# Kernel optimization log

Measured on AMD Instinct MI355X. Metric: run time of the kernel, lower is better.

## Reference

```python
import jax, jax.numpy as jnp
import numpy as np


def setup_inputs() -> dict:
    key = jax.random.key(0)
    ks = jax.random.split(key, 7)
    O, I, K = 64, 64, 3
    D = K * K
    x = jax.random.normal(ks[0], (32, I, 224, 224), jnp.float32)
    weight_loc = jax.random.normal(ks[1], (O, I, K, K), jnp.float32) * 0.05
    weight_L = jax.random.normal(ks[2], (O, I, D, D), jnp.float32) * 0.05
    bias_loc = jax.random.normal(ks[3], (O,), jnp.float32) * 0.05
    bias_ro = jax.random.normal(ks[4], (O,), jnp.float32) * 0.05
    eps_w = jax.random.normal(ks[5], (O, I, D), jnp.float32)
    eps_b = jax.random.normal(ks[6], (O,), jnp.float32)
    return {"x": x, "weight_loc": weight_loc, "weight_L": weight_L,
            "bias_loc": bias_loc, "bias_ro": bias_ro,
            "eps_w": eps_w, "eps_b": eps_b}


def reference(x, weight_loc, weight_L, bias_loc, bias_ro, eps_w, eps_b):
    # weight_loc: [O, I, K, K]; weight_L: [O, I, D, D] with D = K*K
    O, I, K, _ = weight_loc.shape
    D = K * K
    # diag_softplus: softplus on the diagonal of each per-(o,i) scale_tril,
    # keep strictly-lower part; MVN uses the lower-triangular scale_tril.
    diag = jnp.diagonal(weight_L, axis1=-2, axis2=-1)            # [O, I, D]
    eye = jnp.eye(D, dtype=weight_L.dtype)
    L = jnp.tril(weight_L, -1) + jax.nn.softplus(diag)[..., None] * eye  # [O, I, D, D]
    # Batched MVN rsample: loc + L @ eps, collapsing the O*I Python loop
    w = weight_loc + jnp.einsum('oiab,oib->oia', L, eps_w).reshape(O, I, K, K)
    # Bias rsample: loc + eps * softplus(ro)
    b = bias_loc + eps_b * jax.nn.softplus(bias_ro)              # [O]
    out = jax.lax.conv_general_dilated(
        x, w, window_strides=(1, 1), padding='SAME',
        dimension_numbers=('NCHW', 'OIHW', 'NCHW'))
    return out + b[None, :, None, None]
```

## Files before the change

### kernel.cpp

```cpp
#include <hip/hip_runtime.h>
#include <hip/hip_bf16.h>
#include <stdint.h>

typedef short bhalf8 __attribute__((ext_vector_type(8)));
typedef float facc4 __attribute__((ext_vector_type(4)));

static __device__ __forceinline__ unsigned short f2bfu(float f) {
  return __builtin_bit_cast(unsigned short, __float2bfloat16(f));
}

__global__ void prep_kernel(const float* __restrict__ wloc,
                            const float* __restrict__ wL,
                            const float* __restrict__ eps_w,
                            const float* __restrict__ bloc,
                            const float* __restrict__ bro,
                            const float* __restrict__ eps_b,
                            short* __restrict__ wt, float* __restrict__ bias,
                            short* __restrict__ zeros) {
  int t = blockIdx.x * 256 + threadIdx.x;
  int o = t >> 6, i = t & 63;
  int kc = i >> 5, il = i & 31;
  const float* Lp = wL + (size_t)t * 81;
  const float* ep = eps_w + (size_t)t * 9;
  const float* lp = wloc + (size_t)t * 9;
  float e[9];
#pragma unroll
  for (int b = 0; b < 9; ++b) e[b] = ep[b];
#pragma unroll
  for (int a = 0; a < 9; ++a) {
    float s = lp[a];
    for (int b = 0; b < a; ++b) s += Lp[a * 9 + b] * e[b];
    float d = Lp[a * 9 + a];
    float sp = (d > 20.f) ? d : log1pf(expf(d));
    s += sp * e[a];
    wt[((a * 2 + kc) * 64 + o) * 32 + il] = (short)f2bfu(s);
  }
  if (t < 64) {
    float d = bro[t];
    float sp = (d > 20.f) ? d : log1pf(expf(d));
    bias[t] = bloc[t] + eps_b[t] * sp;
  }
  if (t < 16) zeros[t] = 0;
}

__global__ __launch_bounds__(512) void to_nhwc_kernel(
    const float* __restrict__ x, short* __restrict__ xh) {
  int b = blockIdx.x;
  int n = b / 196;
  int p0 = (b % 196) * 256;
  int t = threadIdx.x;
  int pl = t >> 3, c8 = t & 7;
  const float* xp = x + (size_t)(n * 64 + c8 * 8) * 50176 + p0 + pl * 4;
  short* op = xh + ((size_t)n * 50176 + p0 + pl * 4) * 64 + c8 * 8;
  float4 v[8];
#pragma unroll
  for (int j = 0; j < 8; ++j) v[j] = *(const float4*)(xp + (size_t)j * 50176);
#pragma unroll
  for (int s = 0; s < 4; ++s) {
    bhalf8 h;
#pragma unroll
    for (int j = 0; j < 8; ++j) h[j] = f2bfu(((const float*)&v[j])[s]);
    *(bhalf8*)(op + s * 64) = h;
  }
}

__global__ __launch_bounds__(512, 4) void conv_awt_kernel(
    const short* __restrict__ xh, const short* __restrict__ wtg,
    const float* __restrict__ bias, const short* __restrict__ zeros,
    float* __restrict__ out) {
  extern __shared__ short smem[];
  short* lds_x = smem;
  short* lds_w = smem + 21120;

  int b0 = blockIdx.x;
  int b = (b0 & 7) * 448 + (b0 >> 3);
  int ht = b % 28;
  int rest = b / 28;
  int w4 = rest & 3, n = rest >> 2;
  int h0 = ht * 8, w0 = w4 * 64;
  int t = threadIdx.x, lane = t & 63, wv = t >> 6;
  int l15 = lane & 15, l4 = lane >> 4;

  facc4 acc[4][4];
#pragma unroll
  for (int om = 0; om < 4; ++om)
#pragma unroll
    for (int p = 0; p < 4; ++p) {
      facc4 z = {0.f, 0.f, 0.f, 0.f};
      acc[om][p] = z;
    }

  const size_t nbase = (size_t)n * 50176 * 64;
  for (int ic = 0; ic < 2; ++ic) {
#pragma unroll
    for (int k = 0; k < 6; ++k) {
      int id = k * 512 + t;
      if (id < 2640) {
        int cc = id % 66;
        int rg = id / 66;
        int g = rg & 3, r = rg >> 2;
        int h_in = h0 - 1 + r, w_in = w0 - 1 + cc;
        const short* src =
            (h_in >= 0 && h_in < 224 && w_in >= 0 && w_in < 224)
                ? xh + nbase + (size_t)(h_in * 224 + w_in) * 64 + ic * 32 +
                      g * 8
                : zeros;
        __builtin_amdgcn_global_load_lds(
            (const __attribute__((address_space(1))) void*)src,
            (__attribute__((address_space(3))) void*)((char*)lds_x +
                                                      (k * 512 + wv * 64) *
                                                          16),
            16, 0, 0);
      }
    }
#pragma unroll
    for (int k = 0; k < 5; ++k) {
      int w = k * 512 + t;
      if (w < 2304) {
        const short* src = wtg + (w >> 8) * 4096 + ic * 2048 + (w & 255) * 8;
        __builtin_amdgcn_global_load_lds(
            (const __attribute__((address_space(1))) void*)src,
            (__attribute__((address_space(3))) void*)((char*)lds_w +
                                                      (k * 512 + wv * 64) *
                                                          16),
            16, 0, 0);
      }
    }
    __syncthreads();
#pragma unroll
    for (int kh = 0; kh < 3; ++kh) {
      int r = wv + kh;
#pragma unroll
      for (int kw = 0; kw < 3; ++kw) {
        const int tap = kh * 3 + kw;
        const short* ab = lds_w + tap * 2048 + l15 * 32 + (l4 << 3);
        bhalf8 a[4];
#pragma unroll
        for (int om = 0; om < 4; ++om)
          a[om] = *(const bhalf8*)(ab + om * 512);
#pragma unroll
        for (int p = 0; p < 4; ++p) {
          int tc = p * 16 + l15 + kw;
          bhalf8 bv = *(const bhalf8*)(lds_x + (((r * 4 + l4) * 66) + tc) * 8);
#pragma unroll
          for (int om = 0; om < 4; ++om)
            acc[om][p] = __builtin_amdgcn_mfma_f32_16x16x32_bf16(
                a[om], bv, acc[om][p], 0, 0, 0);
        }
      }
    }
    if (ic == 0) __syncthreads();
  }

  int h = h0 + wv;
#pragma unroll
  for (int om = 0; om < 4; ++om) {
#pragma unroll
    for (int jj = 0; jj < 4; ++jj) {
      int o = om * 16 + l4 * 4 + jj;
      float bo = bias[o];
      float* op = out + ((size_t)(n * 64 + o) * 224 + h) * 224 + w0;
#pragma unroll
      for (int p = 0; p < 4; ++p) {
        int wg = w0 + p * 16 + l15;
        if (wg < 224) op[p * 16 + l15] = acc[om][p][jj] + bo;
      }
    }
  }
}

typedef unsigned int uintv2 __attribute__((ext_vector_type(2)));
#define LD1(cj, i)                                                   \
  ((hok && (w_in0 + (i)) >= 0 && (w_in0 + (i)) < 224)                \
       ? cbase[(size_t)(cj) * 50176 + w_in0 + (i)]                   \
       : 0.f)

__global__ __launch_bounds__(256, 4) void conv_onepass_kernel(
    const float* __restrict__ x, const short* __restrict__ wt,
    const float* __restrict__ bias, float* __restrict__ out) {
  __shared__ short lds[6 * 66 * 32];
  int b0 = blockIdx.x;
  int b = (b0 & 7) * 896 + (b0 >> 3);
  int ht = b % 56;
  int rest = b / 56;
  int w4 = rest & 3, n = rest >> 2;
  int h0 = ht * 4, w0 = w4 * 64;
  int t = threadIdx.x, lane = t & 63, wv = t >> 6;
  int l15 = lane & 15, l4 = lane >> 4;

  facc4 acc[4][4];
#pragma unroll
  for (int om = 0; om < 4; ++om)
#pragma unroll
    for (int p = 0; p < 4; ++p) {
      facc4 z = {0.f, 0.f, 0.f, 0.f};
      acc[om][p] = z;
    }

  for (int ic = 0; ic < 2; ++ic) {
#pragma unroll
    for (int k = 0; k < 4; ++k) {
      int u = t + k * 256;
      if (u < 816) {
        int chg = u & 7;
        int tmp = u >> 3;
        int ccg = tmp % 17, r = tmp / 17;
        int h_in = h0 - 1 + r;
        bool hok = (h_in >= 0) & (h_in < 224);
        int w_in0 = w0 - 1 + ccg * 4;
        int ch0 = ic * 32 + chg * 4;
        const float* cbase =
            x + ((size_t)(n * 64 + ch0) * 224 + (hok ? h_in : 0)) * 224;
        float4 v0, v1, v2, v3;
        if (hok && w_in0 >= 0 && w_in0 + 3 < 224) {
          v0 = *(const float4*)(cbase + w_in0);
          v1 = *(const float4*)(cbase + 50176 + w_in0);
          v2 = *(const float4*)(cbase + 2 * 50176 + w_in0);
          v3 = *(const float4*)(cbase + 3 * 50176 + w_in0);
        } else {
          v0 = make_float4(LD1(0, 0), LD1(0, 1), LD1(0, 2), LD1(0, 3));
          v1 = make_float4(LD1(1, 0), LD1(1, 1), LD1(1, 2), LD1(1, 3));
          v2 = make_float4(LD1(2, 0), LD1(2, 1), LD1(2, 2), LD1(2, 3));
          v3 = make_float4(LD1(3, 0), LD1(3, 1), LD1(3, 2), LD1(3, 3));
        }
        int g = chg >> 1;
        int halfsel = (chg & 1) << 2;
#pragma unroll
        for (int i = 0; i < 4; ++i) {
          int cc = ccg * 4 + i;
          if (cc < 66) {
            float a0 = ((const float*)&v0)[i], a1 = ((const float*)&v1)[i];
            float a2 = ((const float*)&v2)[i], a3 = ((const float*)&v3)[i];
            unsigned int w0p =
                (unsigned int)f2bfu(a0) | ((unsigned int)f2bfu(a1) << 16);
            unsigned int w1p =
                (unsigned int)f2bfu(a2) | ((unsigned int)f2bfu(a3) << 16);
            int addr =
                (r * 66 + cc) * 32 + ((g ^ ((cc >> 1) & 3)) << 3) + halfsel;
            uintv2 pk = {w0p, w1p};
            *(uintv2*)(lds + addr) = pk;
          }
        }
      }
    }
    __syncthreads();
#pragma unroll
    for (int kh = 0; kh < 3; ++kh) {
      int r = wv + kh;
#pragma unroll
      for (int kw = 0; kw < 3; ++kw) {
        const short* wb =
            wt + (((kh * 3 + kw) * 2 + ic) * 64 + l15) * 32 + (l4 << 3);
        bhalf8 a[4];
#pragma unroll
        for (int om = 0; om < 4; ++om)
          a[om] = *(const bhalf8*)(wb + om * 512);
#pragma unroll
        for (int p = 0; p < 4; ++p) {
          int tc = p * 16 + l15 + kw;
          bhalf8 bv = *(const bhalf8*)(lds + (r * 66 + tc) * 32 +
                                       ((l4 ^ ((tc >> 1) & 3)) << 3));
#pragma unroll
          for (int om = 0; om < 4; ++om)
            acc[om][p] = __builtin_amdgcn_mfma_f32_16x16x32_bf16(
                a[om], bv, acc[om][p], 0, 0, 0);
        }
      }
    }
    if (ic == 0) __syncthreads();
  }

  int h = h0 + wv;
#pragma unroll
  for (int om = 0; om < 4; ++om) {
#pragma unroll
    for (int j = 0; j < 4; ++j) {
      int o = om * 16 + l4 * 4 + j;
      float bo = bias[o];
      float* op = out + ((size_t)(n * 64 + o) * 224 + h) * 224 + w0;
#pragma unroll
      for (int p = 0; p < 4; ++p) {
        int wg = w0 + p * 16 + l15;
        if (wg < 224) op[p * 16 + l15] = acc[om][p][j] + bo;
      }
    }
  }
}

extern "C" void kernel_launch(void* const* d_in, const int* in_sizes, int n_in,
                              void* d_out, int out_size, void* d_ws,
                              size_t ws_size, hipStream_t stream) {
  const float* x = (const float*)d_in[0];
  const float* wloc = (const float*)d_in[1];
  const float* wL = (const float*)d_in[2];
  const float* bloc = (const float*)d_in[3];
  const float* bro = (const float*)d_in[4];
  const float* eps_w = (const float*)d_in[5];
  const float* eps_b = (const float*)d_in[6];
  float* outp = (float*)d_out;

  short* wt = (short*)d_ws;
  float* bias = (float*)((char*)d_ws + 73728);
  short* zeros = (short*)((char*)d_ws + 73984);
  short* xh = (short*)((char*)d_ws + 74240);
  const size_t need = 74240ull + (size_t)32 * 50176 * 64 * 2;

  prep_kernel<<<16, 256, 0, stream>>>(wloc, wL, eps_w, bloc, bro, eps_b, wt,
                                      bias, zeros);
  if (ws_size >= need) {
    to_nhwc_kernel<<<32 * 196, 512, 0, stream>>>(x, xh);
    const int dyn_lds = (21120 + 18432) * 2;
    hipFuncSetAttribute((const void*)conv_awt_kernel,
                        hipFuncAttributeMaxDynamicSharedMemorySize, dyn_lds);
    conv_awt_kernel<<<3584, 512, dyn_lds, stream>>>(xh, wt, bias, zeros, outp);
  } else {
    conv_onepass_kernel<<<7168, 256, 0, stream>>>(x, wt, bias, outp);
  }
}
```

Measured before the change: 343.6 us.

## Double-buffer conv input/weight staging in LDS across four channel chunks

```diff
diff --git a/kernel.cpp b/kernel.cpp
--- a/kernel.cpp
+++ b/kernel.cpp
@@ -3,6 +3,7 @@
 #include <stdint.h>
 
 typedef short bhalf8 __attribute__((ext_vector_type(8)));
+typedef short bhalf4 __attribute__((ext_vector_type(4)));
 typedef float facc4 __attribute__((ext_vector_type(4)));
 
 static __device__ __forceinline__ unsigned short f2bfu(float f) {
@@ -19,7 +20,6 @@
                             short* __restrict__ zeros) {
   int t = blockIdx.x * 256 + threadIdx.x;
   int o = t >> 6, i = t & 63;
-  int kc = i >> 5, il = i & 31;
   const float* Lp = wL + (size_t)t * 81;
   const float* ep = eps_w + (size_t)t * 9;
   const float* lp = wloc + (size_t)t * 9;
@@ -33,7 +33,7 @@
     float d = Lp[a * 9 + a];
     float sp = (d > 20.f) ? d : log1pf(expf(d));
     s += sp * e[a];
-    wt[((a * 2 + kc) * 64 + o) * 32 + il] = (short)f2bfu(s);
+    wt[((a * 8 + (i >> 3)) * 64 + o) * 8 + (i & 7)] = (short)f2bfu(s);
   }
   if (t < 64) {
     float d = bro[t];
@@ -64,7 +64,7 @@
   }
 }
 
-__global__ __launch_bounds__(512, 4) void conv_awt_kernel(
+__global__ __launch_bounds__(512, 4) void conv_pipe_kernel(
     const short* __restrict__ xh, const short* __restrict__ wtg,
     const float* __restrict__ bias, const short* __restrict__ zeros,
     float* __restrict__ out) {
@@ -80,6 +80,59 @@
   int h0 = ht * 8, w0 = w4 * 64;
   int t = threadIdx.x, lane = t & 63, wv = t >> 6;
   int l15 = lane & 15, l4 = lane >> 4;
+  int gA = l4 >> 1, sub4 = (l4 & 1) * 4;
+
+  const int cxbase = wv * 165;
+  const int cwbase = wv * 144;
+  int pre_px[3];
+#pragma unroll
+  for (int k = 0; k < 3; ++k) {
+    int id = cxbase + k * 64 + lane;
+    if (id >= 1320) id = 0;
+    int cc = id % 66;
+    int rg = id / 66;
+    int g = rg & 1, r = rg >> 1;
+    int h_in = h0 - 1 + r, w_in = w0 - 1 + cc;
+    bool ok = (h_in >= 0) & (h_in < 224) & (w_in >= 0) & (w_in < 224);
+    pre_px[k] = ok ? ((h_in * 224 + w_in) * 64 + g * 8) : -1;
+  }
+  int pre_wt[3];
+#pragma unroll
+  for (int k = 0; k < 3; ++k) {
+    int id = cwbase + k * 64 + lane;
+    if (id >= 1152) id = 0;
+    int a = id >> 7, rem = id & 127;
+    int g = rem >> 6, o = rem & 63;
+    pre_wt[k] = (a * 512 + g * 64 + o) * 8;
+  }
+  const size_t nbase = (size_t)n * 50176 * 64;
+
+#define STAGE(qq)                                                          \
+  do {                                                                     \
+    const int q_ = (qq);                                                   \
+    const short* gx_ = xh + nbase + q_ * 16;                               \
+    short* lx_ = lds_x + (q_ & 1) * 10560 + cxbase * 8;                    \
+    _Pragma("unroll") for (int k = 0; k < 3; ++k) {                        \
+      if (k * 64 + lane < 165) {                                           \
+        const short* src = (pre_px[k] >= 0) ? gx_ + pre_px[k] : zeros;     \
+        __builtin_amdgcn_global_load_lds(                                  \
+            (const __attribute__((address_space(1))) void*)src,            \
+            (__attribute__((address_space(3))) void*)(lx_ + k * 512), 16,  \
+            0, 0);                                                         \
+      }                                                                    \
+    }                                                                      \
+    const short* gw_ = wtg + q_ * 1024;                                    \
+    short* lw_ = lds_w + (q_ & 1) * 9216 + cwbase * 8;                     \
+    _Pragma("unroll") for (int k = 0; k < 3; ++k) {                        \
+      if (k * 64 + lane < 144) {                                           \
+        __builtin_amdgcn_global_load_lds(                                  \
+            (const __attribute__((address_space(1))) void*)(gw_ +          \
+                                                            pre_wt[k]),    \
+            (__attribute__((address_space(3))) void*)(lw_ + k * 512), 16,  \
+            0, 0);                                                         \
+      }                                                                    \
+    }                                                                      \
+  } while (0)
 
   facc4 acc[4][4];
 #pragma unroll
@@ -90,67 +143,49 @@
       acc[om][p] = z;
     }
 
-  const size_t nbase = (size_t)n * 50176 * 64;
-  for (int ic = 0; ic < 2; ++ic) {
-#pragma unroll
-    for (int k = 0; k < 6; ++k) {
-      int id = k * 512 + t;
-      if (id < 2640) {
-        int cc = id % 66;
-        int rg = id / 66;
-        int g = rg & 3, r = rg >> 2;
-        int h_in = h0 - 1 + r, w_in = w0 - 1 + cc;
-        const short* src =
-            (h_in >= 0 && h_in < 224 && w_in >= 0 && w_in < 224)
-                ? xh + nbase + (size_t)(h_in * 224 + w_in) * 64 + ic * 32 +
-                      g * 8
-                : zeros;
-        __builtin_amdgcn_global_load_lds(
-            (const __attribute__((address_space(1))) void*)src,
-            (__attribute__((address_space(3))) void*)((char*)lds_x +
-                                                      (k * 512 + wv * 64) *
-                                                          16),
-            16, 0, 0);
-      }
-    }
-#pragma unroll
-    for (int k = 0; k < 5; ++k) {
-      int w = k * 512 + t;
-      if (w < 2304) {
-        const short* src = wtg + (w >> 8) * 4096 + ic * 2048 + (w & 255) * 8;
-        __builtin_amdgcn_global_load_lds(
-            (const __attribute__((address_space(1))) void*)src,
-            (__attribute__((address_space(3))) void*)((char*)lds_w +
-                                                      (k * 512 + wv * 64) *
-                                                          16),
-            16, 0, 0);
-      }
-    }
-    __syncthreads();
+  STAGE(0);
+#pragma unroll
+  for (int q = 0; q < 4; ++q) {
+    if (q < 3) STAGE(q + 1);
+    __builtin_amdgcn_sched_barrier(0);
+    if (q < 3)
+      asm volatile("s_waitcnt vmcnt(6)" ::: "memory");
+    else
+      asm volatile("s_waitcnt vmcnt(0)" ::: "memory");
+    __builtin_amdgcn_sched_barrier(0);
+    __builtin_amdgcn_s_barrier();
+    __builtin_amdgcn_sched_barrier(0);
+
+    const short* bx = lds_x + (q & 1) * 10560;
+    const short* bw = lds_w + (q & 1) * 9216;
 #pragma unroll
     for (int kh = 0; kh < 3; ++kh) {
       int r = wv + kh;
 #pragma unroll
       for (int kw = 0; kw < 3; ++kw) {
-        const int tap = kh * 3 + kw;
-        const short* ab = lds_w + tap * 2048 + l15 * 32 + (l4 << 3);
-        bhalf8 a[4];
+        const int a = kh * 3 + kw;
+        bhalf4 av[4];
 #pragma unroll
         for (int om = 0; om < 4; ++om)
-          a[om] = *(const bhalf8*)(ab + om * 512);
+          av[om] = *(const bhalf4*)(bw + ((a * 2 + gA) * 64 + om * 16 + l15) *
+                                             8 +
+                                    sub4);
 #pragma unroll
         for (int p = 0; p < 4; ++p) {
           int tc = p * 16 + l15 + kw;
-          bhalf8 bv = *(const bhalf8*)(lds_x + (((r * 4 + l4) * 66) + tc) * 8);
+          bhalf4 bv =
+              *(const bhalf4*)(bx + ((r * 2 + gA) * 66 + tc) * 8 + sub4);
 #pragma unroll
           for (int om = 0; om < 4; ++om)
-            acc[om][p] = __builtin_amdgcn_mfma_f32_16x16x32_bf16(
-                a[om], bv, acc[om][p], 0, 0, 0);
+            acc[om][p] = __builtin_amdgcn_mfma_f32_16x16x16bf16_1k(
+                av[om], bv, acc[om][p], 0, 0, 0);
         }
       }
     }
-    if (ic == 0) __syncthreads();
-  }
+    __builtin_amdgcn_s_barrier();
+    __builtin_amdgcn_sched_barrier(0);
+  }
+#undef STAGE
 
   int h = h0 + wv;
 #pragma unroll
@@ -249,12 +284,13 @@
       int r = wv + kh;
 #pragma unroll
       for (int kw = 0; kw < 3; ++kw) {
-        const short* wb =
-            wt + (((kh * 3 + kw) * 2 + ic) * 64 + l15) * 32 + (l4 << 3);
+        const int tap = kh * 3 + kw;
         bhalf8 a[4];
 #pragma unroll
         for (int om = 0; om < 4; ++om)
-          a[om] = *(const bhalf8*)(wb + om * 512);
+          a[om] = *(const bhalf8*)(wt + ((tap * 8 + ic * 4 + l4) * 64 +
+                                         om * 16 + l15) *
+                                            8);
 #pragma unroll
         for (int p = 0; p < 4; ++p) {
           int tc = p * 16 + l15 + kw;
@@ -310,9 +346,10 @@
   if (ws_size >= need) {
     to_nhwc_kernel<<<32 * 196, 512, 0, stream>>>(x, xh);
     const int dyn_lds = (21120 + 18432) * 2;
-    hipFuncSetAttribute((const void*)conv_awt_kernel,
+    hipFuncSetAttribute((const void*)conv_pipe_kernel,
                         hipFuncAttributeMaxDynamicSharedMemorySize, dyn_lds);
-    conv_awt_kernel<<<3584, 512, dyn_lds, stream>>>(xh, wt, bias, zeros, outp);
+    conv_pipe_kernel<<<3584, 512, dyn_lds, stream>>>(xh, wt, bias, zeros,
+                                                     outp);
   } else {
     conv_onepass_kernel<<<7168, 256, 0, stream>>>(x, wt, bias, outp);
   }
```

After: 393.7 us. +14.6%, slower.
